# Kernel tuning notes

Hardware: AMD Instinct MI355X
Metric: run time of the kernel (lower is better)

## Reference

```python
import jax, jax.numpy as jnp
import numpy as np

H, LMAX, NSEG, EPS = 8, 2, 16, 1e-7
S = (LMAX + 1) ** 2  # 9 spherical components
L_OF_M = jnp.asarray(np.floor(np.sqrt(np.arange(S))).astype(np.int32))  # degree l of each m-component


def so3_linear(x, W, b):
    # x [n,S,Cin]; W [LMAX+1,Cin,Cout] per-degree weights; bias only on l=0 (invariant) component
    y = jnp.einsum('nsi,sio->nso', x, W[L_OF_M])
    return y + b[None, None, :] * (jnp.arange(S) == 0)[None, :, None]


def equiv_layernorm(x, gamma, beta):
    # x [N,S,C]; standard LN on l=0 scalars, RMS-of-irrep-norm scaling (equivariant) for l>0
    x0 = x[:, 0, :]
    mu = jnp.mean(x0, -1, keepdims=True)
    var = jnp.mean((x0 - mu) ** 2, -1, keepdims=True)
    outs = [(((x0 - mu) / jnp.sqrt(var + EPS)) * gamma[0] + beta)[:, None, :]]
    for l in range(1, LMAX + 1):
        xl = x[:, l * l:(l + 1) * (l + 1), :]               # [N,2l+1,C]
        n2 = jnp.mean(xl * xl, axis=1)                      # [N,C] mean sq over m
        rms = jnp.sqrt(jnp.mean(n2, -1, keepdims=True) + EPS)  # [N,1]
        outs.append(xl / rms[:, None, :] * gamma[l][None, None, :])
    return jnp.concatenate(outs, axis=1)


def setup_inputs() -> dict:
    key = jax.random.key(0)
    ks = jax.random.split(key, 12)
    N, E, CIN, CH = 512, 8192, 128, 256
    return dict(
        q=jax.random.normal(ks[0], (N, S, CIN), jnp.float32),
        k=jax.random.normal(ks[1], (N, S, CIN), jnp.float32),
        v=jax.random.normal(ks[2], (N, S, CIN), jnp.float32),
        envelope=jax.random.uniform(ks[3], (E,), jnp.float32),
        attn_bias=jax.random.normal(ks[4], (H, E), jnp.float32),
        atom_index=jax.random.randint(ks[5], (E,), 0, N),
        batch_index=jnp.sort(jax.random.randint(ks[6], (E,), 0, NSEG)),
        edge_map_tab=jax.random.randint(ks[7], (E,), 0, E),
        Wq=jax.random.normal(ks[8], (LMAX + 1, CIN, CH), jnp.float32) / np.float32(np.sqrt(CIN)),
        bq=jnp.zeros((CH,), jnp.float32),
        Wk=jax.random.normal(ks[9], (LMAX + 1, CIN, CH), jnp.float32) / np.float32(np.sqrt(CIN)),
        bk=jnp.zeros((CH,), jnp.float32),
        Wv=jax.random.normal(ks[10], (LMAX + 1, CIN, CH), jnp.float32) / np.float32(np.sqrt(CIN)),
        bv=jnp.zeros((CH,), jnp.float32),
        gamma=jnp.ones((LMAX + 1, CH), jnp.float32),
        beta=jnp.zeros((CH,), jnp.float32),
        Wo=jax.random.normal(ks[11], (LMAX + 1, CH, CIN), jnp.float32) / np.float32(np.sqrt(CH)),
        bo=jnp.zeros((CIN,), jnp.float32),
    )


def reference(q, k, v, envelope, attn_bias, atom_index, batch_index, edge_map_tab,
              Wq, bq, Wk, bk, Wv, bv, gamma, beta, Wo, bo):
    N, E = q.shape[0], atom_index.shape[0]
    qh = so3_linear(q, Wq, bq)                      # [N,S,CH]
    kh = so3_linear(k, Wk, bk)[atom_index]          # [E,S,CH] gather per edge
    vh = so3_linear(v, Wv, bv)[atom_index]
    CH = qh.shape[-1]
    d = CH // H
    qh = qh.reshape(N, S, H, d).transpose(2, 0, 1, 3).reshape(H, N, S * d)
    kh = kh.reshape(E, S, H, d).transpose(2, 0, 1, 3).reshape(H, E, S * d)
    vh = vh.reshape(E, S, H, d).transpose(2, 0, 1, 3).reshape(H, E, S * d)
    scale = np.float32(np.sqrt(d / 3.0) / d)
    scores = jnp.einsum('hnf,hef->hne', qh * scale, kh)         # [H,N,E]
    scores = scores + attn_bias[:, edge_map_tab][:, None, :]
    env_e = envelope[edge_map_tab]                               # [E]
    # smooth scatter softmax grouped by batch_index over edge axis
    st = scores.transpose(2, 0, 1)                               # [E,H,N]
    mx = jax.ops.segment_max(st, batch_index, num_segments=NSEG)
    rec = jnp.exp(st - mx[batch_index]) * env_e[:, None, None]
    den = jax.ops.segment_sum(rec, batch_index, num_segments=NSEG)
    attn = rec / (den[batch_index] + 1e-16)
    attn = (attn * env_e[:, None, None]).transpose(1, 2, 0)      # [H,N,E]
    out = jnp.einsum('hne,hef->hnf', attn, vh)                   # [H,N,S*d]
    out = out.transpose(1, 0, 2).reshape(N, H, S, d).transpose(0, 2, 1, 3).reshape(N, S, CH)
    out = equiv_layernorm(out, gamma, beta)
    return so3_linear(out, Wo, bo)
```

## Files before the change

kernel.cpp:

```cpp
#include <hip/hip_runtime.h>
#include <hip/hip_bf16.h>
#include <math.h>

#define NH 8
#define SDIM 9
#define NSEG 16
#define NATOM 512
#define NEDGE 8192
#define CIN 128
#define CHN 256
#define DH 32
#define FDIM 288
#define EPS 1e-7f
#define SCALE 0.10206207261596577f

typedef __attribute__((ext_vector_type(8))) short bf16x8;
typedef __attribute__((ext_vector_type(8))) short short8;
typedef __attribute__((ext_vector_type(4))) float f32x4;

__device__ inline float blockReduceMax(float v, float* red) {
    #pragma unroll
    for (int off = 32; off; off >>= 1) v = fmaxf(v, __shfl_xor(v, off, 64));
    int lane = threadIdx.x & 63, wid = threadIdx.x >> 6;
    if (lane == 0) red[wid] = v;
    __syncthreads();
    v = fmaxf(fmaxf(red[0], red[1]), fmaxf(red[2], red[3]));
    __syncthreads();
    return v;
}
__device__ inline int lower_bound_batch(const int* __restrict__ b, int val) {
    int lo = 0, hi = NEDGE;
    while (lo < hi) {
        int mid = (lo + hi) >> 1;
        if (b[mid] < val) lo = mid + 1; else hi = mid;
    }
    return lo;
}
__device__ inline ushort f2bu(float x) {
    __hip_bfloat16 b = __float2bfloat16(x);
    return *(ushort*)&b;
}

__global__ void __launch_bounds__(256) stage1(const int* __restrict__ batch,
                                              const int* __restrict__ am, const int* __restrict__ emap,
                                              const float* __restrict__ envelope,
                                              const float* __restrict__ attn_bias,
                                              float* __restrict__ E1, float* __restrict__ E2,
                                              const float* __restrict__ q, const float* __restrict__ k,
                                              const float* __restrict__ v,
                                              const float* __restrict__ Wq, const float* __restrict__ Wk,
                                              const float* __restrict__ Wv,
                                              const float* __restrict__ bq, const float* __restrict__ bk,
                                              const float* __restrict__ bv,
                                              ushort* __restrict__ qhB,
                                              ushort* __restrict__ khB,
                                              ushort* __restrict__ vhT,
                                              const float* __restrict__ Wo,
                                              ushort* __restrict__ WoT,
                                              float* __restrict__ stats) {
    const int bid = blockIdx.x;
    const int tid = threadIdx.x;
    if (bid < NSEG * NH) {
        const int seg = bid & (NSEG - 1), h = bid >> 4;
        __shared__ float e1[NATOM];
        __shared__ float e2[NATOM];
        __shared__ float red[4];
        e1[tid] = 0.f; e1[tid + 256] = 0.f;
        e2[tid] = 0.f; e2[tid + 256] = 0.f;
        const float* bh = attn_bias + (size_t)h * NEDGE;
        float mv = -1e30f;
        for (int e = tid; e < NEDGE; e += 256) mv = fmaxf(mv, bh[e]);
        const float mb = blockReduceMax(mv, red);
        const int st = lower_bound_batch(batch, seg);
        const int en = lower_bound_batch(batch, seg + 1);
        for (int e = st + tid; e < en; e += 256) {
            int m = am[e], em = emap[e];
            float ev = envelope[em];
            float eb = __expf(bh[em] - mb);
            atomicAdd(&e1[m], ev * eb);
            atomicAdd(&e2[m], ev * ev * eb);
        }
        __syncthreads();
        size_t base = ((size_t)h * NSEG + seg) * NATOM;
        E1[base + tid] = e1[tid]; E1[base + tid + 256] = e1[tid + 256];
        E2[base + tid] = e2[tid]; E2[base + tid + 256] = e2[tid + 256];
        return;
    }
    if (bid < NSEG * NH + 48) {
        const int t = bid - NSEG * NH;
        const int l = t / 16;
        const int cb = (t & 15) >> 2, ob = t & 3;
        const int c0 = cb * 64, o0 = ob * 32;
        __shared__ float tile[64][33];
        const float* src = Wo + (size_t)l * CHN * CIN;
        #pragma unroll
        for (int p = 0; p < 8; ++p) {
            int row = p * 8 + (tid >> 5);
            int col = tid & 31;
            tile[row][col] = src[(size_t)(c0 + row) * CIN + o0 + col];
        }
        __syncthreads();
        ushort* dst = WoT + (size_t)l * CIN * CHN;
        #pragma unroll
        for (int p = 0; p < 8; ++p) {
            int o = p * 4 + (tid >> 6);
            int c = tid & 63;
            dst[(size_t)(o0 + o) * CHN + c0 + c] = f2bu(tile[c][o]);
        }
        return;
    }
    if (bid < NSEG * NH + 48 + 432) {
        const int idx = bid - (NSEG * NH + 48);
        const int z = idx / 144;
        const int rem = idx - z * 144;
        const int s = rem >> 4;
        const int n0 = (rem & 15) * 32;
        const int l = (s == 0) ? 0 : ((s < 4) ? 1 : 2);
        const float* x = (z == 0) ? q : (z == 1) ? k : v;
        const float* W = ((z == 0) ? Wq : (z == 1) ? Wk : Wv) + (size_t)l * CIN * CHN;
        const float* bias = (z == 0) ? bq : (z == 1) ? bk : bv;
        const int lane = tid & 63, w = tid >> 6;
        const int wr = w >> 1, wc = w & 1;
        const int r = lane & 15, kg = lane >> 4;
        const int arow = n0 + 16 * wr + r;
        const float* xrow = x + ((size_t)arow * SDIM + s) * CIN;
        f32x4 acc[8] = {};
        #pragma unroll
        for (int ks = 0; ks < 4; ++ks) {
            const int k0 = ks * 32 + kg * 8;
            float4 x0 = *(const float4*)(xrow + k0);
            float4 x1 = *(const float4*)(xrow + k0 + 4);
            bf16x8 a;
            a[0] = f2bu(x0.x); a[1] = f2bu(x0.y); a[2] = f2bu(x0.z); a[3] = f2bu(x0.w);
            a[4] = f2bu(x1.x); a[5] = f2bu(x1.y); a[6] = f2bu(x1.z); a[7] = f2bu(x1.w);
            #pragma unroll
            for (int j = 0; j < 8; ++j) {
                const int o = 128 * wc + 16 * j + r;
                const float* wp = W + (size_t)k0 * CHN + o;
                bf16x8 bf;
                #pragma unroll
                for (int jj = 0; jj < 8; ++jj) bf[jj] = f2bu(wp[(size_t)jj * CHN]);
                acc[j] = __builtin_amdgcn_mfma_f32_16x16x32_bf16(a, bf, acc[j], 0, 0, 0);
            }
        }
        const float sc = (z == 0) ? SCALE : 1.0f;
        #pragma unroll
        for (int j = 0; j < 8; ++j) {
            const int o = 128 * wc + 16 * j + r;
            const float bb = (s == 0) ? bias[o] : 0.f;
            const int h = o >> 5, dj = o & 31;
            const int f = s * DH + dj;
            if (z < 2) {
                ushort* dst = (z == 0) ? qhB : khB;
                #pragma unroll
                for (int p = 0; p < 4; ++p) {
                    int row = n0 + 16 * wr + kg * 4 + p;
                    dst[((size_t)h * NATOM + row) * FDIM + f] = f2bu((acc[j][p] + bb) * sc);
                }
            } else {
                ushort* dst = vhT + ((size_t)h * FDIM + f) * NATOM;
                #pragma unroll
                for (int p = 0; p < 4; ++p) {
                    int row = n0 + 16 * wr + kg * 4 + p;
                    dst[row] = f2bu(acc[j][p] + bb);
                }
            }
        }
        return;
    }
    {
        float4 z4 = {0.f, 0.f, 0.f, 0.f};
        float4* sp = (float4*)stats;
        sp[tid] = z4;
        sp[tid + 256] = z4;
    }
}

__global__ void __launch_bounds__(256) attn_fused(const ushort* __restrict__ qhB,
                                                  const ushort* __restrict__ khB,
                                                  const float* __restrict__ E1,
                                                  const float* __restrict__ E2,
                                                  ushort* __restrict__ attnB) {
    const int h = blockIdx.y;
    const int n0 = blockIdx.x * 16;
    __shared__ float E1s[NSEG][NATOM];
    __shared__ float E2s[NSEG][NATOM];
    __shared__ float rowmax[4][16];
    __shared__ float Dpart[4][16][NSEG];
    __shared__ float invDs[16][NSEG];
    const int tid = threadIdx.x;
    const int lane = tid & 63, w = tid >> 6;
    const int r = lane & 15, kg = lane >> 4;
    {
        const float* e1g = E1 + (size_t)h * NSEG * NATOM;
        const float* e2g = E2 + (size_t)h * NSEG * NATOM;
        for (int i = tid * 4; i < NSEG * NATOM; i += 1024) {
            *(float4*)&((float*)E1s)[i] = *(const float4*)&e1g[i];
            *(float4*)&((float*)E2s)[i] = *(const float4*)&e2g[i];
        }
    }
    const ushort* A = qhB + (size_t)h * NATOM * FDIM;
    const ushort* B = khB + (size_t)h * NATOM * FDIM;
    const int ar = n0 + r;
    f32x4 acc[8] = {};
    #pragma unroll
    for (int ks = 0; ks < FDIM / 32; ++ks) {
        const int k0 = ks * 32 + kg * 8;
        bf16x8 a = *(const bf16x8*)(A + (size_t)ar * FDIM + k0);
        #pragma unroll
        for (int j = 0; j < 8; ++j) {
            const int bcol = w * 128 + 16 * j + r;
            bf16x8 b = *(const bf16x8*)(B + (size_t)bcol * FDIM + k0);
            acc[j] = __builtin_amdgcn_mfma_f32_16x16x32_bf16(a, b, acc[j], 0, 0, 0);
        }
    }
    __syncthreads();
    float pm[4];
    #pragma unroll
    for (int p = 0; p < 4; ++p) {
        float m = acc[0][p];
        #pragma unroll
        for (int j = 1; j < 8; ++j) m = fmaxf(m, acc[j][p]);
        pm[p] = m;
    }
    #pragma unroll
    for (int mk = 1; mk < 16; mk <<= 1)
        #pragma unroll
        for (int p = 0; p < 4; ++p) pm[p] = fmaxf(pm[p], __shfl_xor(pm[p], mk, 64));
    if (r == 0) {
        #pragma unroll
        for (int p = 0; p < 4; ++p) rowmax[w][kg * 4 + p] = pm[p];
    }
    __syncthreads();
    float mx[4];
    #pragma unroll
    for (int p = 0; p < 4; ++p) {
        int row = kg * 4 + p;
        mx[p] = fmaxf(fmaxf(rowmax[0][row], rowmax[1][row]),
                      fmaxf(rowmax[2][row], rowmax[3][row]));
    }
    float es[8][4];
    #pragma unroll
    for (int j = 0; j < 8; ++j)
        #pragma unroll
        for (int p = 0; p < 4; ++p) es[j][p] = __expf(acc[j][p] - mx[p]);
    float Dp[4][NSEG] = {};
    #pragma unroll
    for (int j = 0; j < 8; ++j) {
        const int col = w * 128 + 16 * j + r;
        #pragma unroll
        for (int g = 0; g < NSEG; ++g) {
            float e1 = E1s[g][col];
            #pragma unroll
            for (int p = 0; p < 4; ++p) Dp[p][g] += es[j][p] * e1;
        }
    }
    #pragma unroll
    for (int mk = 1; mk < 16; mk <<= 1)
        #pragma unroll
        for (int p = 0; p < 4; ++p)
            #pragma unroll
            for (int g = 0; g < NSEG; ++g) Dp[p][g] += __shfl_xor(Dp[p][g], mk, 64);
    if (r == 0) {
        #pragma unroll
        for (int p = 0; p < 4; ++p)
            #pragma unroll
            for (int g = 0; g < NSEG; ++g) Dpart[w][kg * 4 + p][g] = Dp[p][g];
    }
    __syncthreads();
    {
        int row = tid >> 4, g = tid & 15;
        float d = Dpart[0][row][g] + Dpart[1][row][g] + Dpart[2][row][g] + Dpart[3][row][g];
        invDs[row][g] = 1.0f / (d + 1e-30f);
    }
    __syncthreads();
    float iv[4][NSEG];
    #pragma unroll
    for (int p = 0; p < 4; ++p)
        #pragma unroll
        for (int g = 0; g < NSEG; ++g) iv[p][g] = invDs[kg * 4 + p][g];
    ushort* sbuf = (ushort*)E1s;
    #pragma unroll
    for (int j = 0; j < 8; ++j) {
        const int col = w * 128 + 16 * j + r;
        float ww[4] = {};
        #pragma unroll
        for (int g = 0; g < NSEG; ++g) {
            float e2 = E2s[g][col];
            #pragma unroll
            for (int p = 0; p < 4; ++p) ww[p] += e2 * iv[p][g];
        }
        #pragma unroll
        for (int p = 0; p < 4; ++p)
            sbuf[(kg * 4 + p) * NATOM + col] = f2bu(es[j][p] * ww[p]);
    }
    __syncthreads();
    {
        ushort* dst = attnB + ((size_t)h * NATOM + n0) * NATOM;
        for (int i = tid * 8; i < 16 * NATOM; i += 2048)
            *(short8*)(dst + i) = *(short8*)(sbuf + i);
    }
}

__global__ void __launch_bounds__(256) gemm_out_stats(const ushort* __restrict__ attnB,
                                                      const ushort* __restrict__ vhT,
                                                      float* __restrict__ attnOut,
                                                      float* __restrict__ stats) {
    const int h = blockIdx.z;
    const int fb = blockIdx.x;
    const int n0 = blockIdx.y * 64;
    const int tid = threadIdx.x;
    const int lane = tid & 63, w = tid >> 6;
    const int r = lane & 15, kg = lane >> 4;
    const ushort* A = attnB + (size_t)h * NATOM * NATOM;
    const ushort* B = vhT + (size_t)h * FDIM * NATOM;
    const int ar = n0 + 16 * w + r;
    f32x4 acc[2] = {};
    #pragma unroll 4
    for (int ks = 0; ks < NATOM / 32; ++ks) {
        const int k0 = ks * 32 + kg * 8;
        bf16x8 a = *(const bf16x8*)(A + (size_t)ar * NATOM + k0);
        bf16x8 b0 = *(const bf16x8*)(B + (size_t)(32 * fb + 16 * 0 + r) * NATOM + k0);
        bf16x8 b1 = *(const bf16x8*)(B + (size_t)(32 * fb + 16 * 1 + r) * NATOM + k0);
        acc[0] = __builtin_amdgcn_mfma_f32_16x16x32_bf16(a, b0, acc[0], 0, 0, 0);
        acc[1] = __builtin_amdgcn_mfma_f32_16x16x32_bf16(a, b1, acc[1], 0, 0, 0);
    }
    float sA[4], sB[4];
    #pragma unroll
    for (int p = 0; p < 4; ++p) { sA[p] = 0.f; sB[p] = 0.f; }
    #pragma unroll
    for (int j = 0; j < 2; ++j) {
        const int dj = 16 * j + r;
        #pragma unroll
        for (int p = 0; p < 4; ++p) {
            const int row = n0 + 16 * w + kg * 4 + p;
            float x = acc[j][p];
            attnOut[((size_t)row * SDIM + fb) * CHN + h * DH + dj] = x;
            sA[p] += x;
            sB[p] += x * x;
        }
    }
    #pragma unroll
    for (int mk = 1; mk < 16; mk <<= 1)
        #pragma unroll
        for (int p = 0; p < 4; ++p) {
            sA[p] += __shfl_xor(sA[p], mk, 64);
            sB[p] += __shfl_xor(sB[p], mk, 64);
        }
    if (r == 0) {
        #pragma unroll
        for (int p = 0; p < 4; ++p) {
            const int row = n0 + 16 * w + kg * 4 + p;
            if (fb == 0) {
                atomicAdd(&stats[row * 4 + 0], sA[p]);
                atomicAdd(&stats[row * 4 + 1], sB[p]);
            } else if (fb < 4) {
                atomicAdd(&stats[row * 4 + 2], sB[p]);
            } else {
                atomicAdd(&stats[row * 4 + 3], sB[p]);
            }
        }
    }
}

__global__ void __launch_bounds__(256) so3out_ln(const float* __restrict__ attnOut,
                                                 const float* __restrict__ stats,
                                                 const float* __restrict__ gamma,
                                                 const float* __restrict__ beta,
                                                 const ushort* __restrict__ WoT,
                                                 const float* __restrict__ bo,
                                                 float* __restrict__ out) {
    const int s = blockIdx.y;
    const int n0 = blockIdx.x * 16;
    const int l = (s == 0) ? 0 : ((s < 4) ? 1 : 2);
    const int tid = threadIdx.x;
    const int lane = tid & 63, w = tid >> 6;
    const int r = lane & 15, kg = lane >> 4;
    const int ar = n0 + r;
    float mu, ivl;
    {
        float s0 = stats[ar * 4 + 0];
        float q0 = stats[ar * 4 + 1];
        float q1 = stats[ar * 4 + 2];
        float q2 = stats[ar * 4 + 3];
        float m0 = s0 * (1.0f / CHN);
        float var = q0 * (1.0f / CHN) - m0 * m0;
        if (s == 0) { mu = m0; ivl = 1.0f / sqrtf(var + EPS); }
        else if (s < 4) { mu = 0.f; ivl = 1.0f / sqrtf(q1 * (1.0f / (3 * CHN)) + EPS); }
        else { mu = 0.f; ivl = 1.0f / sqrtf(q2 * (1.0f / (5 * CHN)) + EPS); }
    }
    const float* xrow = attnOut + ((size_t)ar * SDIM + s) * CHN;
    const float* gl = gamma + l * CHN;
    const ushort* B = WoT + (size_t)l * CIN * CHN;
    f32x4 acc[2] = {};
    #pragma unroll
    for (int ks = 0; ks < CHN / 32; ++ks) {
        const int k0 = ks * 32 + kg * 8;
        float4 x0 = *(const float4*)(xrow + k0);
        float4 x1 = *(const float4*)(xrow + k0 + 4);
        float4 g0 = *(const float4*)(gl + k0);
        float4 g1 = *(const float4*)(gl + k0 + 4);
        float y[8];
        y[0] = (x0.x - mu) * ivl * g0.x; y[1] = (x0.y - mu) * ivl * g0.y;
        y[2] = (x0.z - mu) * ivl * g0.z; y[3] = (x0.w - mu) * ivl * g0.w;
        y[4] = (x1.x - mu) * ivl * g1.x; y[5] = (x1.y - mu) * ivl * g1.y;
        y[6] = (x1.z - mu) * ivl * g1.z; y[7] = (x1.w - mu) * ivl * g1.w;
        if (s == 0) {
            float4 b0 = *(const float4*)(beta + k0);
            float4 b1 = *(const float4*)(beta + k0 + 4);
            y[0] += b0.x; y[1] += b0.y; y[2] += b0.z; y[3] += b0.w;
            y[4] += b1.x; y[5] += b1.y; y[6] += b1.z; y[7] += b1.w;
        }
        bf16x8 a;
        #pragma unroll
        for (int jj = 0; jj < 8; ++jj) a[jj] = f2bu(y[jj]);
        bf16x8 b0f = *(const bf16x8*)(B + (size_t)(32 * w + 16 * 0 + r) * CHN + k0);
        bf16x8 b1f = *(const bf16x8*)(B + (size_t)(32 * w + 16 * 1 + r) * CHN + k0);
        acc[0] = __builtin_amdgcn_mfma_f32_16x16x32_bf16(a, b0f, acc[0], 0, 0, 0);
        acc[1] = __builtin_amdgcn_mfma_f32_16x16x32_bf16(a, b1f, acc[1], 0, 0, 0);
    }
    #pragma unroll
    for (int j = 0; j < 2; ++j) {
        const int o = 32 * w + 16 * j + r;
        const float badd = (s == 0) ? bo[o] : 0.f;
        #pragma unroll
        for (int p = 0; p < 4; ++p) {
            const int n = n0 + kg * 4 + p;
            out[((size_t)n * SDIM + s) * CIN + o] = acc[j][p] + badd;
        }
    }
}

extern "C" void kernel_launch(void* const* d_in, const int* in_sizes, int n_in,
                              void* d_out, int out_size, void* d_ws, size_t ws_size,
                              hipStream_t stream) {
    const float* q = (const float*)d_in[0];
    const float* k = (const float*)d_in[1];
    const float* v = (const float*)d_in[2];
    const float* envelope = (const float*)d_in[3];
    const float* attn_bias = (const float*)d_in[4];
    const int* atom_index = (const int*)d_in[5];
    const int* batch_index = (const int*)d_in[6];
    const int* edge_map = (const int*)d_in[7];
    const float* Wq = (const float*)d_in[8];
    const float* bq = (const float*)d_in[9];
    const float* Wk = (const float*)d_in[10];
    const float* bk = (const float*)d_in[11];
    const float* Wv = (const float*)d_in[12];
    const float* bv = (const float*)d_in[13];
    const float* gamma = (const float*)d_in[14];
    const float* beta = (const float*)d_in[15];
    const float* Wo = (const float*)d_in[16];
    const float* bo = (const float*)d_in[17];
    float* out = (float*)d_out;

    const size_t SZ_HNF = (size_t)NH * NATOM * FDIM;
    const size_t SZ_HNN = (size_t)NH * NATOM * NATOM;
    const size_t SZ_TAB = (size_t)NH * NSEG * NATOM;
    const size_t SZ_WOT = (size_t)3 * CIN * CHN;
    const size_t SZ_NSC = (size_t)NATOM * SDIM * CHN;

    char* wsb = (char*)d_ws;
    ushort* qhB = (ushort*)wsb;
    ushort* khB = qhB + SZ_HNF;
    ushort* vhT = khB + SZ_HNF;
    ushort* attnB = vhT + SZ_HNF;
    float* attnOut = (float*)(attnB + SZ_HNN);
    float* E1 = attnOut + SZ_NSC;
    float* E2 = E1 + SZ_TAB;
    ushort* WoT = (ushort*)(E2 + SZ_TAB);
    float* stats = (float*)(WoT + SZ_WOT);

    size_t needed = 2 * 3 * SZ_HNF + 2 * SZ_HNN + 4 * SZ_NSC + 4 * 2 * SZ_TAB
                  + 2 * SZ_WOT + 4 * NATOM * 4 + 256;
    if (ws_size < needed) return;

    stage1<<<NSEG * NH + 48 + 432 + 1, 256, 0, stream>>>(
        batch_index, atom_index, edge_map, envelope, attn_bias, E1, E2,
        q, k, v, Wq, Wk, Wv, bq, bk, bv, qhB, khB, vhT, Wo, WoT, stats);
    attn_fused<<<dim3(NATOM / 16, NH), 256, 0, stream>>>(qhB, khB, E1, E2, attnB);
    gemm_out_stats<<<dim3(SDIM, NATOM / 64, NH), 256, 0, stream>>>(attnB, vhT, attnOut, stats);
    so3out_ln<<<dim3(NATOM / 16, SDIM), 256, 0, stream>>>(attnOut, stats, gamma, beta, WoT, bo, out);
}
```

Baseline: 74.72 us.

## Fuse attention-weighted V GEMM into attention kernel and pre-transpose QKV weights

```diff
diff --git a/kernel.cpp b/kernel.cpp
--- a/kernel.cpp
+++ b/kernel.cpp
@@ -41,6 +41,47 @@
     return *(ushort*)&b;
 }
 
+__global__ void __launch_bounds__(256) wtrans(const float* __restrict__ Wq, const float* __restrict__ Wk,
+                                              const float* __restrict__ Wv, const float* __restrict__ Wo,
+                                              ushort* __restrict__ WqT, ushort* __restrict__ WkT,
+                                              ushort* __restrict__ WvT, ushort* __restrict__ WoT) {
+    const int bid = blockIdx.x;
+    const int tid = threadIdx.x;
+    __shared__ float tile[64][33];
+    const float* src; ushort* dst; int R, C, r0, c0;
+    if (bid < 144) {
+        const int z = bid / 48;
+        const int rem = bid % 48;
+        const int l = rem >> 4;
+        const int t = rem & 15;
+        R = CIN; C = CHN;
+        r0 = (t >> 3) * 64; c0 = (t & 7) * 32;
+        src = ((z == 0) ? Wq : (z == 1) ? Wk : Wv) + (size_t)l * R * C;
+        dst = ((z == 0) ? WqT : (z == 1) ? WkT : WvT) + (size_t)l * R * C;
+    } else {
+        const int rem = bid - 144;
+        const int l = rem >> 4;
+        const int t = rem & 15;
+        R = CHN; C = CIN;
+        r0 = (t >> 2) * 64; c0 = (t & 3) * 32;
+        src = Wo + (size_t)l * R * C;
+        dst = WoT + (size_t)l * R * C;
+    }
+    #pragma unroll
+    for (int p = 0; p < 8; ++p) {
+        int row = p * 8 + (tid >> 5);
+        int col = tid & 31;
+        tile[row][col] = src[(size_t)(r0 + row) * C + c0 + col];
+    }
+    __syncthreads();
+    #pragma unroll
+    for (int p = 0; p < 8; ++p) {
+        int c = p * 4 + (tid >> 6);
+        int rr = tid & 63;
+        dst[(size_t)(c0 + c) * R + r0 + rr] = f2bu(tile[rr][c]);
+    }
+}
+
 __global__ void __launch_bounds__(256) stage1(const int* __restrict__ batch,
                                               const int* __restrict__ am, const int* __restrict__ emap,
                                               const float* __restrict__ envelope,
@@ -48,15 +89,13 @@
                                               float* __restrict__ E1, float* __restrict__ E2,
                                               const float* __restrict__ q, const float* __restrict__ k,
                                               const float* __restrict__ v,
-                                              const float* __restrict__ Wq, const float* __restrict__ Wk,
-                                              const float* __restrict__ Wv,
+                                              const ushort* __restrict__ WqT, const ushort* __restrict__ WkT,
+                                              const ushort* __restrict__ WvT,
                                               const float* __restrict__ bq, const float* __restrict__ bk,
                                               const float* __restrict__ bv,
                                               ushort* __restrict__ qhB,
                                               ushort* __restrict__ khB,
                                               ushort* __restrict__ vhT,
-                                              const float* __restrict__ Wo,
-                                              ushort* __restrict__ WoT,
                                               float* __restrict__ stats) {
     const int bid = blockIdx.x;
     const int tid = threadIdx.x;
@@ -86,38 +125,15 @@
         E2[base + tid] = e2[tid]; E2[base + tid + 256] = e2[tid + 256];
         return;
     }
-    if (bid < NSEG * NH + 48) {
-        const int t = bid - NSEG * NH;
-        const int l = t / 16;
-        const int cb = (t & 15) >> 2, ob = t & 3;
-        const int c0 = cb * 64, o0 = ob * 32;
-        __shared__ float tile[64][33];
-        const float* src = Wo + (size_t)l * CHN * CIN;
-        #pragma unroll
-        for (int p = 0; p < 8; ++p) {
-            int row = p * 8 + (tid >> 5);
-            int col = tid & 31;
-            tile[row][col] = src[(size_t)(c0 + row) * CIN + o0 + col];
-        }
-        __syncthreads();
-        ushort* dst = WoT + (size_t)l * CIN * CHN;
-        #pragma unroll
-        for (int p = 0; p < 8; ++p) {
-            int o = p * 4 + (tid >> 6);
-            int c = tid & 63;
-            dst[(size_t)(o0 + o) * CHN + c0 + c] = f2bu(tile[c][o]);
-        }
-        return;
-    }
-    if (bid < NSEG * NH + 48 + 432) {
-        const int idx = bid - (NSEG * NH + 48);
+    if (bid < NSEG * NH + 432) {
+        const int idx = bid - NSEG * NH;
         const int z = idx / 144;
         const int rem = idx - z * 144;
         const int s = rem >> 4;
         const int n0 = (rem & 15) * 32;
         const int l = (s == 0) ? 0 : ((s < 4) ? 1 : 2);
         const float* x = (z == 0) ? q : (z == 1) ? k : v;
-        const float* W = ((z == 0) ? Wq : (z == 1) ? Wk : Wv) + (size_t)l * CIN * CHN;
+        const ushort* WT = ((z == 0) ? WqT : (z == 1) ? WkT : WvT) + (size_t)l * CIN * CHN;
         const float* bias = (z == 0) ? bq : (z == 1) ? bk : bv;
         const int lane = tid & 63, w = tid >> 6;
         const int wr = w >> 1, wc = w & 1;
@@ -136,10 +152,7 @@
             #pragma unroll
             for (int j = 0; j < 8; ++j) {
                 const int o = 128 * wc + 16 * j + r;
-                const float* wp = W + (size_t)k0 * CHN + o;
-                bf16x8 bf;
-                #pragma unroll
-                for (int jj = 0; jj < 8; ++jj) bf[jj] = f2bu(wp[(size_t)jj * CHN]);
+                bf16x8 bf = *(const bf16x8*)(WT + (size_t)o * CIN + k0);
                 acc[j] = __builtin_amdgcn_mfma_f32_16x16x32_bf16(a, bf, acc[j], 0, 0, 0);
             }
         }
@@ -176,11 +189,14 @@
     }
 }
 
-__global__ void __launch_bounds__(256) attn_fused(const ushort* __restrict__ qhB,
-                                                  const ushort* __restrict__ khB,
-                                                  const float* __restrict__ E1,
-                                                  const float* __restrict__ E2,
-                                                  ushort* __restrict__ attnB) {
+#define SBST 520
+__global__ void __launch_bounds__(256) attn_out_fused(const ushort* __restrict__ qhB,
+                                                      const ushort* __restrict__ khB,
+                                                      const ushort* __restrict__ vhT,
+                                                      const float* __restrict__ E1,
+                                                      const float* __restrict__ E2,
+                                                      float* __restrict__ attnOut,
+                                                      float* __restrict__ stats) {
     const int h = blockIdx.y;
     const int n0 = blockIdx.x * 16;
     __shared__ float E1s[NSEG][NATOM];
@@ -292,73 +308,50 @@
         }
         #pragma unroll
         for (int p = 0; p < 4; ++p)
-            sbuf[(kg * 4 + p) * NATOM + col] = f2bu(es[j][p] * ww[p]);
-    }
-    __syncthreads();
-    {
-        ushort* dst = attnB + ((size_t)h * NATOM + n0) * NATOM;
-        for (int i = tid * 8; i < 16 * NATOM; i += 2048)
-            *(short8*)(dst + i) = *(short8*)(sbuf + i);
-    }
-}
-
-__global__ void __launch_bounds__(256) gemm_out_stats(const ushort* __restrict__ attnB,
-                                                      const ushort* __restrict__ vhT,
-                                                      float* __restrict__ attnOut,
-                                                      float* __restrict__ stats) {
-    const int h = blockIdx.z;
-    const int fb = blockIdx.x;
-    const int n0 = blockIdx.y * 64;
-    const int tid = threadIdx.x;
-    const int lane = tid & 63, w = tid >> 6;
-    const int r = lane & 15, kg = lane >> 4;
-    const ushort* A = attnB + (size_t)h * NATOM * NATOM;
-    const ushort* B = vhT + (size_t)h * FDIM * NATOM;
-    const int ar = n0 + 16 * w + r;
-    f32x4 acc[2] = {};
-    #pragma unroll 4
-    for (int ks = 0; ks < NATOM / 32; ++ks) {
-        const int k0 = ks * 32 + kg * 8;
-        bf16x8 a = *(const bf16x8*)(A + (size_t)ar * NATOM + k0);
-        bf16x8 b0 = *(const bf16x8*)(B + (size_t)(32 * fb + 16 * 0 + r) * NATOM + k0);
-        bf16x8 b1 = *(const bf16x8*)(B + (size_t)(32 * fb + 16 * 1 + r) * NATOM + k0);
-        acc[0] = __builtin_amdgcn_mfma_f32_16x16x32_bf16(a, b0, acc[0], 0, 0, 0);
-        acc[1] = __builtin_amdgcn_mfma_f32_16x16x32_bf16(a, b1, acc[1], 0, 0, 0);
-    }
-    float sA[4], sB[4];
-    #pragma unroll
-    for (int p = 0; p < 4; ++p) { sA[p] = 0.f; sB[p] = 0.f; }
-    #pragma unroll
-    for (int j = 0; j < 2; ++j) {
-        const int dj = 16 * j + r;
+            sbuf[(kg * 4 + p) * SBST + col] = f2bu(es[j][p] * ww[p]);
+    }
+    __syncthreads();
+    const ushort* Bv = vhT + (size_t)h * FDIM * NATOM;
+    float S0[4] = {}, Q0[4] = {}, Q1[4] = {}, Q2[4] = {};
+    for (int fc = w; fc < FDIM / 16; fc += 4) {
+        const int f0 = fc * 16;
+        f32x4 oacc = {};
+        #pragma unroll
+        for (int ks = 0; ks < NATOM / 32; ++ks) {
+            const int k0 = ks * 32 + kg * 8;
+            bf16x8 a = *(const bf16x8*)(sbuf + r * SBST + k0);
+            bf16x8 b = *(const bf16x8*)(Bv + (size_t)(f0 + r) * NATOM + k0);
+            oacc = __builtin_amdgcn_mfma_f32_16x16x32_bf16(a, b, oacc, 0, 0, 0);
+        }
+        const int f = f0 + r;
+        const int s = f >> 5, dj = f & 31;
         #pragma unroll
         for (int p = 0; p < 4; ++p) {
-            const int row = n0 + 16 * w + kg * 4 + p;
-            float x = acc[j][p];
-            attnOut[((size_t)row * SDIM + fb) * CHN + h * DH + dj] = x;
-            sA[p] += x;
-            sB[p] += x * x;
+            const int row = n0 + kg * 4 + p;
+            float x = oacc[p];
+            attnOut[((size_t)row * SDIM + s) * CHN + h * DH + dj] = x;
+            if (s == 0) { S0[p] += x; Q0[p] += x * x; }
+            else if (s < 4) Q1[p] += x * x;
+            else Q2[p] += x * x;
         }
     }
     #pragma unroll
     for (int mk = 1; mk < 16; mk <<= 1)
         #pragma unroll
         for (int p = 0; p < 4; ++p) {
-            sA[p] += __shfl_xor(sA[p], mk, 64);
-            sB[p] += __shfl_xor(sB[p], mk, 64);
+            S0[p] += __shfl_xor(S0[p], mk, 64);
+            Q0[p] += __shfl_xor(Q0[p], mk, 64);
+            Q1[p] += __shfl_xor(Q1[p], mk, 64);
+            Q2[p] += __shfl_xor(Q2[p], mk, 64);
         }
     if (r == 0) {
         #pragma unroll
         for (int p = 0; p < 4; ++p) {
-            const int row = n0 + 16 * w + kg * 4 + p;
-            if (fb == 0) {
-                atomicAdd(&stats[row * 4 + 0], sA[p]);
-                atomicAdd(&stats[row * 4 + 1], sB[p]);
-            } else if (fb < 4) {
-                atomicAdd(&stats[row * 4 + 2], sB[p]);
-            } else {
-                atomicAdd(&stats[row * 4 + 3], sB[p]);
-            }
+            const int row = n0 + kg * 4 + p;
+            atomicAdd(&stats[row * 4 + 0], S0[p]);
+            atomicAdd(&stats[row * 4 + 1], Q0[p]);
+            atomicAdd(&stats[row * 4 + 2], Q1[p]);
+            atomicAdd(&stats[row * 4 + 3], Q2[p]);
         }
     }
 }
@@ -455,7 +448,6 @@
     float* out = (float*)d_out;
 
     const size_t SZ_HNF = (size_t)NH * NATOM * FDIM;
-    const size_t SZ_HNN = (size_t)NH * NATOM * NATOM;
     const size_t SZ_TAB = (size_t)NH * NSEG * NATOM;
     const size_t SZ_WOT = (size_t)3 * CIN * CHN;
     const size_t SZ_NSC = (size_t)NATOM * SDIM * CHN;
@@ -464,21 +456,25 @@
     ushort* qhB = (ushort*)wsb;
     ushort* khB = qhB + SZ_HNF;
     ushort* vhT = khB + SZ_HNF;
-    ushort* attnB = vhT + SZ_HNF;
-    float* attnOut = (float*)(attnB + SZ_HNN);
+    float* attnOut = (float*)(vhT + SZ_HNF);
     float* E1 = attnOut + SZ_NSC;
     float* E2 = E1 + SZ_TAB;
-    ushort* WoT = (ushort*)(E2 + SZ_TAB);
+    ushort* WqT = (ushort*)(E2 + SZ_TAB);
+    ushort* WkT = WqT + SZ_WOT;
+    ushort* WvT = WkT + SZ_WOT;
+    ushort* WoT = WvT + SZ_WOT;
     float* stats = (float*)(WoT + SZ_WOT);
 
-    size_t needed = 2 * 3 * SZ_HNF + 2 * SZ_HNN + 4 * SZ_NSC + 4 * 2 * SZ_TAB
-                  + 2 * SZ_WOT + 4 * NATOM * 4 + 256;
+    size_t needed = 2 * 3 * SZ_HNF + 4 * SZ_NSC + 4 * 2 * SZ_TAB
+                  + 2 * 4 * SZ_WOT + 4 * NATOM * 4 + 256;
     if (ws_size < needed) return;
 
-    stage1<<<NSEG * NH + 48 + 432 + 1, 256, 0, stream>>>(
+    wtrans<<<192, 256, 0, stream>>>(Wq, Wk, Wv, Wo, WqT, WkT, WvT, WoT);
+    stage1<<<NSEG * NH + 432 + 1, 256, 0, stream>>>(
         batch_index, atom_index, edge_map, envelope, attn_bias, E1, E2,
-        q, k, v, Wq, Wk, Wv, bq, bk, bv, qhB, khB, vhT, Wo, WoT, stats);
-    attn_fused<<<dim3(NATOM / 16, NH), 256, 0, stream>>>(qhB, khB, E1, E2, attnB);
-    gemm_out_stats<<<dim3(SDIM, NATOM / 64, NH), 256, 0, stream>>>(attnB, vhT, attnOut, stats);
-    so3out_ln<<<dim3(NATOM / 16, SDIM), 256, 0, stream>>>(attnOut, stats, gamma, beta, WoT, bo, out);
-}
+        q, k, v, WqT, WkT, WvT, bq, bk, bv, qhB, khB, vhT, stats);
+    attn_out_fused<<<dim3(NATOM / 16, NH), 256, 0, stream>>>(
+        qhB, khB, vhT, E1, E2, attnOut, stats);
+    so3out_ln<<<dim3(NATOM / 16, SDIM), 256, 0, stream>>>(
+        attnOut, stats, gamma, beta, WoT, bo, out);
+}
```

Measured after the change: 86.80 us. 16.2% more time.
